# Optimization experiments

Measured on AMD Instinct MI355X. Metric: run time of the kernel, lower is better.

The kernel has to match this reference:

```python
import jax, jax.numpy as jnp
import numpy as np
import math

ROPE_BASE = 10000.0

def _rope(x):
    # x: [B, H, S, D]; interleaved-pair LLaMA-style rotary embedding
    S, D = x.shape[-2], x.shape[-1]
    inv_freq = 1.0 / (ROPE_BASE ** (jnp.arange(0, D, 2, dtype=jnp.float32) / D))  # [D/2]
    ang = jnp.arange(S, dtype=jnp.float32)[:, None] * inv_freq[None, :]           # [S, D/2]
    cos, sin = jnp.cos(ang), jnp.sin(ang)
    x1, x2 = x[..., 0::2], x[..., 1::2]
    r1 = x1 * cos - x2 * sin
    r2 = x1 * sin + x2 * cos
    return jnp.stack([r1, r2], axis=-1).reshape(x.shape)

def setup_inputs() -> dict:
    key = jax.random.key(0)
    ks = jax.random.split(key, 5)
    B, S, E = 2, 2048, 2048
    scale = 1.0 / math.sqrt(E)
    return {
        "x": jax.random.normal(ks[0], (B, S, E), dtype=jnp.float32),
        "Wq": jax.random.normal(ks[1], (E, E), dtype=jnp.float32) * scale,
        "Wk": jax.random.normal(ks[2], (E, E), dtype=jnp.float32) * scale,
        "Wv": jax.random.normal(ks[3], (E, E), dtype=jnp.float32) * scale,
        "Wo": jax.random.normal(ks[4], (E, E), dtype=jnp.float32) * scale,
    }

def reference(x, Wq, Wk, Wv, Wo):
    B, S, E = x.shape
    H = 16
    D = E // H
    # projections (torch Linear: y = x @ W^T, weights stored [out, in])
    def proj(W):
        y = jnp.einsum('bse,oe->bso', x, W)
        return y.reshape(B, S, H, D).transpose(0, 2, 1, 3)  # [B,H,S,D]
    q, k, v = proj(Wq), proj(Wk), proj(Wv)
    q_rot, k_rot = _rope(q), _rope(k)
    scores = jnp.einsum('bhqd,bhkd->bhqk', q_rot, k_rot) / jnp.sqrt(jnp.float32(D))
    causal = jnp.tril(jnp.ones((S, S), dtype=bool))
    scores = jnp.where(causal[None, None], scores, -jnp.inf)
    attn = jax.nn.softmax(scores, axis=-1)
    out = jnp.einsum('bhqk,bhkd->bhqd', attn, v)
    out = out.transpose(0, 2, 1, 3).reshape(B, S, E)
    attn_out = jnp.einsum('bse,oe->bso', out, Wo)
    return (attn_out, k, v)
```

## Files before the change

kernel.cpp:

```cpp
#include <hip/hip_runtime.h>

typedef __attribute__((ext_vector_type(8))) short short8;
typedef __attribute__((ext_vector_type(4))) float floatx4;

#define B_ 2
#define S_ 2048
#define E_ 2048
#define H_ 16
#define D_ 128

#define NEG_S  (-3.0e4f)
#define LOG2E  1.4426950408889634f

__device__ inline float bf2f(unsigned short u) {
    union { unsigned int i; float f; } v; v.i = ((unsigned int)u) << 16; return v.f;
}
__device__ inline unsigned short f2bf(float f) {
    union { float f; unsigned int i; } v; v.f = f;
    unsigned int r = v.i + 0x7FFFu + ((v.i >> 16) & 1u);
    return (unsigned short)(r >> 16);
}

__device__ inline void gload_lds16(const void* g, void* l) {
    __builtin_amdgcn_global_load_lds((__attribute__((address_space(1))) void*)(void*)g,
                                     (__attribute__((address_space(3))) void*)l, 16, 0, 0);
}

__global__ void rope_tab(float* __restrict__ cosT, float* __restrict__ sinT) {
    int idx = blockIdx.x * 256 + threadIdx.x;
    int s = idx >> 6, j = idx & 63;
    float inv = exp2f(-(float)(2 * j) * (13.287712379549449f / 128.0f));
    float ang = (float)s * inv;
    cosT[idx] = cosf(ang);
    sinT[idx] = sinf(ang);
}

__global__ __launch_bounds__(256) void cvt_bf16(const float* __restrict__ in,
                                                unsigned short* __restrict__ out, int n8) {
    int i = blockIdx.x * 256 + threadIdx.x;
    if (i >= n8) return;
    float4 f0 = *(const float4*)(in + (size_t)i * 8);
    float4 f1 = *(const float4*)(in + (size_t)i * 8 + 4);
    unsigned short u[8] = {f2bf(f0.x), f2bf(f0.y), f2bf(f0.z), f2bf(f0.w),
                           f2bf(f1.x), f2bf(f1.y), f2bf(f1.z), f2bf(f1.w)};
    *(uint4*)(out + (size_t)i * 8) = *(uint4*)u;
}

__global__ __launch_bounds__(256) void prep_k(const float* __restrict__ K,
                                              unsigned short* __restrict__ Kr,
                                              const float* __restrict__ cosT,
                                              const float* __restrict__ sinT) {
    int idx = blockIdx.x * 256 + threadIdx.x;
    int g = idx & 15;
    int s = (idx >> 4) & (S_ - 1);
    const float* src = K + (size_t)idx * 8;
    float4 f0 = *(const float4*)src;
    float4 f1 = *(const float4*)(src + 4);
    float xs[8] = {f0.x, f0.y, f0.z, f0.w, f1.x, f1.y, f1.z, f1.w};
    unsigned short u[8];
    int jb = g * 4;
#pragma unroll
    for (int i = 0; i < 4; i++) {
        float c = cosT[s * 64 + jb + i], sn = sinT[s * 64 + jb + i];
        float x1 = xs[2 * i], x2 = xs[2 * i + 1];
        u[2 * i]     = f2bf(x1 * c - x2 * sn);
        u[2 * i + 1] = f2bf(x1 * sn + x2 * c);
    }
    *(uint4*)(Kr + (size_t)idx * 8) = *(uint4*)u;
}

__global__ __launch_bounds__(256) void prep_v(const float* __restrict__ V,
                                              unsigned short* __restrict__ Vt) {
    __shared__ unsigned short Ls[64][130];
    int bh = blockIdx.y;
    int s0 = blockIdx.x * 64;
    int t = threadIdx.x;
    const float* src = V + ((size_t)bh * S_ + s0) * D_;
#pragma unroll
    for (int it = 0; it < 4; it++) {
        int r = it * 16 + (t >> 4), d0 = (t & 15) * 8;
        float4 f0 = *(const float4*)&src[(size_t)r * D_ + d0];
        float4 f1 = *(const float4*)&src[(size_t)r * D_ + d0 + 4];
        unsigned short u[8] = {f2bf(f0.x), f2bf(f0.y), f2bf(f0.z), f2bf(f0.w),
                               f2bf(f1.x), f2bf(f1.y), f2bf(f1.z), f2bf(f1.w)};
#pragma unroll
        for (int i = 0; i < 8; i++) Ls[r][d0 + i] = u[i];
    }
    __syncthreads();
    unsigned short* dst = Vt + (size_t)bh * D_ * S_;
#pragma unroll
    for (int it = 0; it < 4; it++) {
        int d = it * 32 + (t >> 3), ss = (t & 7) * 8;
        unsigned short u[8];
#pragma unroll
        for (int i = 0; i < 8; i++) u[i] = Ls[ss + i][d];
        *(uint4*)&dst[(size_t)d * S_ + s0 + ss] = *(uint4*)u;
    }
}

__global__ __launch_bounds__(256) void gemm128(const unsigned short* __restrict__ A,
                                               const unsigned short* __restrict__ Bw,
                                               void* __restrict__ dst, int dstMode) {
    __shared__ __align__(16) unsigned short As[128][32];
    __shared__ __align__(16) unsigned short Bs[128][32];
    int t = threadIdx.x;
    int wave = t >> 6, lane = t & 63;
    int quad = lane >> 4, l16 = lane & 15;
    int wr = wave >> 1, wc = wave & 1;

    floatx4 acc[4][4];
#pragma unroll
    for (int m = 0; m < 4; m++)
#pragma unroll
        for (int n = 0; n < 4; n++) acc[m][n] = (floatx4)(0.f);

    int srow = lane >> 2;
    int sg = lane & 3;
    const size_t aRow0 = (size_t)blockIdx.x * 128;
    const size_t bRow0 = (size_t)blockIdx.y * 128;

    for (int k0 = 0; k0 < E_; k0 += 32) {
#pragma unroll
        for (int i = 0; i < 2; i++) {
            int lr = wave * 32 + i * 16 + srow;
            int gg = sg ^ ((lr >> 1) & 3);
            gload_lds16(A + (aRow0 + lr) * E_ + k0 + gg * 8, &As[wave * 32 + i * 16][0]);
            gload_lds16(Bw + (bRow0 + lr) * E_ + k0 + gg * 8, &Bs[wave * 32 + i * 16][0]);
        }
        __syncthreads();
        short8 af[4], bfr[4];
#pragma unroll
        for (int m = 0; m < 4; m++) {
            int r = wr * 64 + m * 16 + l16;
            af[m] = *(const short8*)((const char*)As + r * 64 + ((quad ^ ((r >> 1) & 3)) << 4));
        }
#pragma unroll
        for (int n = 0; n < 4; n++) {
            int r = wc * 64 + n * 16 + l16;
            bfr[n] = *(const short8*)((const char*)Bs + r * 64 + ((quad ^ ((r >> 1) & 3)) << 4));
        }
#pragma unroll
        for (int m = 0; m < 4; m++)
#pragma unroll
            for (int n = 0; n < 4; n++)
                acc[m][n] = __builtin_amdgcn_mfma_f32_16x16x32_bf16(af[m], bfr[n], acc[m][n], 0, 0, 0);
        __syncthreads();
    }
#pragma unroll
    for (int m = 0; m < 4; m++)
#pragma unroll
        for (int n = 0; n < 4; n++)
#pragma unroll
            for (int rr = 0; rr < 4; rr++) {
                int mg = (int)aRow0 + wr * 64 + m * 16 + quad * 4 + rr;
                int ng = (int)bRow0 + wc * 64 + n * 16 + l16;
                float val = acc[m][n][rr];
                if (dstMode == 0) {
                    ((float*)dst)[(size_t)mg * E_ + ng] = val;
                } else if (dstMode == 1) {
                    int b = mg >> 11, s = mg & 2047, h = ng >> 7, d = ng & 127;
                    ((float*)dst)[(((size_t)(b * H_ + h)) * S_ + s) * D_ + d] = val;
                } else {
                    ((unsigned short*)dst)[(size_t)mg * E_ + ng] = f2bf(val);
                }
            }
}

__global__ __launch_bounds__(256) void attn_fast(const unsigned short* __restrict__ Qf,
                                                 const unsigned short* __restrict__ Kr,
                                                 const unsigned short* __restrict__ Vt,
                                                 const float* __restrict__ cosT,
                                                 const float* __restrict__ sinT,
                                                 unsigned short* __restrict__ Omid) {
    __shared__ __align__(16) unsigned short Ks[64][128];
    __shared__ __align__(16) unsigned short Vs[128][64];
    __shared__ __align__(16) unsigned short Ps[4][16][72];

    int t = threadIdx.x;
    int wave = t >> 6, lane = t & 63;
    int quad = lane >> 4, l16 = lane & 15;
    int orig = blockIdx.x;
    int L = (orig & 7) * 64 + (orig >> 3);
    int h = L >> 5;
    int qtile = 31 - (L & 31);
    int b = blockIdx.y;

    const unsigned short* Qb = Qf + (size_t)b * S_ * E_;
    const unsigned short* Kh = Kr + ((size_t)(b * H_ + h)) * S_ * D_;
    const unsigned short* Vh = Vt + ((size_t)(b * H_ + h)) * D_ * S_;

    int sq = qtile * 64 + wave * 16 + l16;
    short8 qf[4];
#pragma unroll
    for (int ks = 0; ks < 4; ks++) {
        int d0 = ks * 32 + quad * 8;
        union { uint4 u4; unsigned short u[8]; } un;
        un.u4 = *(const uint4*)&Qb[(size_t)sq * E_ + h * D_ + d0];
#pragma unroll
        for (int i = 0; i < 4; i++) {
            int j = (d0 >> 1) + i;
            float c = cosT[sq * 64 + j], s = sinT[sq * 64 + j];
            float x1 = bf2f(un.u[2 * i]), x2 = bf2f(un.u[2 * i + 1]);
            un.u[2 * i] = f2bf(x1 * c - x2 * s);
            un.u[2 * i + 1] = f2bf(x1 * s + x2 * c);
        }
        qf[ks] = *(short8*)un.u;
    }

    floatx4 O[8];
#pragma unroll
    for (int i = 0; i < 8; i++) O[i] = (floatx4)(0.f);
    float mrow[4], lrow[4];
#pragma unroll
    for (int r = 0; r < 4; r++) { mrow[r] = NEG_S; lrow[r] = 0.f; }

    const float scale = 0.08838834764831845f;

    for (int kt = 0; kt <= qtile; kt++) {
#pragma unroll
        for (int i = 0; i < 4; i++) {
            int r = wave * 16 + i * 4 + (lane >> 4);
            int g = (lane & 15) ^ (r & 7);
            gload_lds16(&Kh[(size_t)(kt * 64 + r) * D_ + g * 8], &Ks[wave * 16 + i * 4][0]);
        }
#pragma unroll
        for (int i = 0; i < 4; i++) {
            int r = wave * 32 + i * 8 + (lane >> 3);
            int g = (lane & 7) ^ (r & 7);
            gload_lds16(&Vh[(size_t)r * S_ + kt * 64 + g * 8], &Vs[wave * 32 + i * 8][0]);
        }
        __syncthreads();

        floatx4 sc[4];
#pragma unroll
        for (int ct = 0; ct < 4; ct++) sc[ct] = (floatx4)(0.f);
#pragma unroll
        for (int ks = 0; ks < 4; ks++) {
#pragma unroll
            for (int ct = 0; ct < 4; ct++) {
                int r = ct * 16 + l16;
                short8 kf = *(const short8*)((const char*)Ks + r * 256 +
                                             ((((ks << 2) + quad) ^ (r & 7)) << 4));
                sc[ct] = __builtin_amdgcn_mfma_f32_16x16x32_bf16(qf[ks], kf, sc[ct], 0, 0, 0);
            }
        }
        int rowbase = qtile * 64 + wave * 16 + quad * 4;
#pragma unroll
        for (int ct = 0; ct < 4; ct++) {
            int col = kt * 64 + ct * 16 + l16;
#pragma unroll
            for (int rr = 0; rr < 4; rr++) {
                float x = sc[ct][rr] * scale;
                sc[ct][rr] = (col > rowbase + rr) ? NEG_S : x;
            }
        }
        float alpha[4];
#pragma unroll
        for (int rr = 0; rr < 4; rr++) {
            float mx = fmaxf(fmaxf(sc[0][rr], sc[1][rr]), fmaxf(sc[2][rr], sc[3][rr]));
            mx = fmaxf(mx, __shfl_xor(mx, 1));
            mx = fmaxf(mx, __shfl_xor(mx, 2));
            mx = fmaxf(mx, __shfl_xor(mx, 4));
            mx = fmaxf(mx, __shfl_xor(mx, 8));
            float mnew = fmaxf(mrow[rr], mx);
            alpha[rr] = exp2f((mrow[rr] - mnew) * LOG2E);
            mrow[rr] = mnew;
        }
#pragma unroll
        for (int rr = 0; rr < 4; rr++) {
            float ps = 0.f;
#pragma unroll
            for (int ct = 0; ct < 4; ct++) {
                float p = exp2f((sc[ct][rr] - mrow[rr]) * LOG2E);
                sc[ct][rr] = p;
                ps += p;
            }
            ps += __shfl_xor(ps, 1);
            ps += __shfl_xor(ps, 2);
            ps += __shfl_xor(ps, 4);
            ps += __shfl_xor(ps, 8);
            lrow[rr] = lrow[rr] * alpha[rr] + ps;
        }
#pragma unroll
        for (int c8 = 0; c8 < 8; c8++)
#pragma unroll
            for (int rr = 0; rr < 4; rr++) O[c8][rr] *= alpha[rr];

#pragma unroll
        for (int ct = 0; ct < 4; ct++)
#pragma unroll
            for (int rr = 0; rr < 4; rr++)
                Ps[wave][quad * 4 + rr][ct * 16 + l16] = f2bf(sc[ct][rr]);
        asm volatile("s_waitcnt lgkmcnt(0)" ::: "memory");
        __builtin_amdgcn_sched_barrier(0);

#pragma unroll
        for (int ka2 = 0; ka2 < 2; ka2++) {
            short8 pa = *(const short8*)&Ps[wave][l16][ka2 * 32 + quad * 8];
#pragma unroll
            for (int c8 = 0; c8 < 8; c8++) {
                int r = c8 * 16 + l16;
                short8 vf = *(const short8*)((const char*)Vs + r * 128 +
                                             ((((ka2 << 2) + quad) ^ (r & 7)) << 4));
                O[c8] = __builtin_amdgcn_mfma_f32_16x16x32_bf16(pa, vf, O[c8], 0, 0, 0);
            }
        }
        asm volatile("s_waitcnt lgkmcnt(0)" ::: "memory");
        __builtin_amdgcn_sched_barrier(0);
        __syncthreads();
    }

#pragma unroll
    for (int rr = 0; rr < 4; rr++) {
        float inv = 1.f / lrow[rr];
        int row = qtile * 64 + wave * 16 + quad * 4 + rr;
#pragma unroll
        for (int c8 = 0; c8 < 8; c8++) {
            int d = c8 * 16 + l16;
            Omid[((size_t)b * S_ + row) * E_ + h * D_ + d] = f2bf(O[c8][rr] * inv);
        }
    }
}


__global__ __launch_bounds__(256) void gemm_bt(const void* __restrict__ A,
                                               const float* __restrict__ Bw,
                                               void* __restrict__ dst,
                                               int aBf16, int dstMode) {
    __shared__ __align__(16) unsigned short As[64][40];
    __shared__ __align__(16) unsigned short Bs[64][40];
    int t = threadIdx.x;
    int wave = t >> 6, lane = t & 63;
    int quad = lane >> 4, l16 = lane & 15;
    floatx4 acc[4];
#pragma unroll
    for (int i = 0; i < 4; i++) acc[i] = (floatx4)(0.f);

    int r = t >> 2, kc = (t & 3) * 8;
    int ra = blockIdx.x * 64 + r;
    int rb = blockIdx.y * 64 + r;

    for (int k0 = 0; k0 < E_; k0 += 32) {
        if (aBf16) {
            const unsigned short* Ab = (const unsigned short*)A + (size_t)ra * E_ + kc + k0;
            *(uint4*)&As[r][kc] = *(const uint4*)Ab;
        } else {
            const float* Af = (const float*)A + (size_t)ra * E_ + kc + k0;
            float4 f0 = *(const float4*)Af;
            float4 f1 = *(const float4*)(Af + 4);
            unsigned short u[8] = {f2bf(f0.x), f2bf(f0.y), f2bf(f0.z), f2bf(f0.w),
                                   f2bf(f1.x), f2bf(f1.y), f2bf(f1.z), f2bf(f1.w)};
            *(uint4*)&As[r][kc] = *(uint4*)u;
        }
        {
            const float* Bf = Bw + (size_t)rb * E_ + kc + k0;
            float4 g0 = *(const float4*)Bf;
            float4 g1 = *(const float4*)(Bf + 4);
            unsigned short u[8] = {f2bf(g0.x), f2bf(g0.y), f2bf(g0.z), f2bf(g0.w),
                                   f2bf(g1.x), f2bf(g1.y), f2bf(g1.z), f2bf(g1.w)};
            *(uint4*)&Bs[r][kc] = *(uint4*)u;
        }
        __syncthreads();
        short8 a = *(const short8*)&As[wave * 16 + l16][quad * 8];
#pragma unroll
        for (int ct = 0; ct < 4; ct++) {
            short8 bfr = *(const short8*)&Bs[ct * 16 + l16][quad * 8];
            acc[ct] = __builtin_amdgcn_mfma_f32_16x16x32_bf16(a, bfr, acc[ct], 0, 0, 0);
        }
        __syncthreads();
    }
#pragma unroll
    for (int ct = 0; ct < 4; ct++) {
#pragma unroll
        for (int rr = 0; rr < 4; rr++) {
            int m = blockIdx.x * 64 + wave * 16 + quad * 4 + rr;
            int n = blockIdx.y * 64 + ct * 16 + l16;
            float val = acc[ct][rr];
            if (dstMode == 0) {
                ((float*)dst)[(size_t)m * E_ + n] = val;
            } else if (dstMode == 1) {
                int b = m >> 11, s = m & 2047, h = n >> 7, d = n & 127;
                ((float*)dst)[(((size_t)(b * H_ + h)) * S_ + s) * D_ + d] = val;
            } else {
                ((unsigned short*)dst)[(size_t)m * E_ + n] = f2bf(val);
            }
        }
    }
}

__global__ __launch_bounds__(256) void attn_fwd(const unsigned short* __restrict__ Qf,
                                                const float* __restrict__ Kb0,
                                                const float* __restrict__ Vb0,
                                                const float* __restrict__ cosT,
                                                const float* __restrict__ sinT,
                                                unsigned short* __restrict__ Omid,
                                                int qtile0) {
    __shared__ __align__(16) unsigned short Ks[64][136];
    __shared__ __align__(16) unsigned short Vt[128][72];
    __shared__ __align__(16) unsigned short Ps[4][16][72];

    int t = threadIdx.x;
    int wave = t >> 6, lane = t & 63;
    int quad = lane >> 4, l16 = lane & 15;
    int qtile = qtile0 + blockIdx.x, h = blockIdx.y;
    const float* Kb = Kb0 + (size_t)h * S_ * D_;
    const float* Vb = Vb0 + (size_t)h * S_ * D_;

    int sq = qtile * 64 + wave * 16 + l16;
    short8 qf[4];
#pragma unroll
    for (int ks = 0; ks < 4; ks++) {
        int d0 = ks * 32 + quad * 8;
        union { uint4 u4; unsigned short u[8]; } un;
        un.u4 = *(const uint4*)&Qf[(size_t)sq * E_ + h * D_ + d0];
#pragma unroll
        for (int i = 0; i < 4; i++) {
            int j = (d0 >> 1) + i;
            float c = cosT[sq * 64 + j], s = sinT[sq * 64 + j];
            float x1 = bf2f(un.u[2 * i]), x2 = bf2f(un.u[2 * i + 1]);
            un.u[2 * i] = f2bf(x1 * c - x2 * s);
            un.u[2 * i + 1] = f2bf(x1 * s + x2 * c);
        }
        qf[ks] = *(short8*)un.u;
    }

    floatx4 O[8];
#pragma unroll
    for (int i = 0; i < 8; i++) O[i] = (floatx4)(0.f);
    float mrow[4], lrow[4];
#pragma unroll
    for (int r = 0; r < 4; r++) { mrow[r] = NEG_S; lrow[r] = 0.f; }

    const float scale = 0.08838834764831845f;

    for (int kt = 0; kt <= qtile; kt++) {
        __syncthreads();
        int r = t >> 2;
#pragma unroll
        for (int it = 0; it < 4; it++) {
            int d0 = (t & 3) * 8 + it * 32;
            int sk = kt * 64 + r;
            float4 ka = *(const float4*)&Kb[(size_t)sk * D_ + d0];
            float4 kb2 = *(const float4*)&Kb[(size_t)sk * D_ + d0 + 4];
            float xs[8] = {ka.x, ka.y, ka.z, ka.w, kb2.x, kb2.y, kb2.z, kb2.w};
            unsigned short u[8];
#pragma unroll
            for (int i = 0; i < 4; i++) {
                int j = (d0 >> 1) + i;
                float c = cosT[sk * 64 + j], s = sinT[sk * 64 + j];
                float x1 = xs[2 * i], x2 = xs[2 * i + 1];
                u[2 * i]     = f2bf(x1 * c - x2 * s);
                u[2 * i + 1] = f2bf(x1 * s + x2 * c);
            }
            *(uint4*)&Ks[r][d0] = *(uint4*)u;
            float4 va = *(const float4*)&Vb[(size_t)sk * D_ + d0];
            float4 vb2 = *(const float4*)&Vb[(size_t)sk * D_ + d0 + 4];
            float vs[8] = {va.x, va.y, va.z, va.w, vb2.x, vb2.y, vb2.z, vb2.w};
#pragma unroll
            for (int i = 0; i < 8; i++) Vt[d0 + i][r] = f2bf(vs[i]);
        }
        __syncthreads();

        floatx4 sc[4];
#pragma unroll
        for (int ct = 0; ct < 4; ct++) sc[ct] = (floatx4)(0.f);
#pragma unroll
        for (int ks = 0; ks < 4; ks++) {
#pragma unroll
            for (int ct = 0; ct < 4; ct++) {
                short8 kf = *(const short8*)&Ks[ct * 16 + l16][ks * 32 + quad * 8];
                sc[ct] = __builtin_amdgcn_mfma_f32_16x16x32_bf16(qf[ks], kf, sc[ct], 0, 0, 0);
            }
        }
        int rowbase = qtile * 64 + wave * 16 + quad * 4;
#pragma unroll
        for (int ct = 0; ct < 4; ct++) {
            int col = kt * 64 + ct * 16 + l16;
#pragma unroll
            for (int rr = 0; rr < 4; rr++) {
                float x = sc[ct][rr] * scale;
                sc[ct][rr] = (col > rowbase + rr) ? NEG_S : x;
            }
        }
        float alpha[4];
#pragma unroll
        for (int rr = 0; rr < 4; rr++) {
            float mx = fmaxf(fmaxf(sc[0][rr], sc[1][rr]), fmaxf(sc[2][rr], sc[3][rr]));
            mx = fmaxf(mx, __shfl_xor(mx, 1));
            mx = fmaxf(mx, __shfl_xor(mx, 2));
            mx = fmaxf(mx, __shfl_xor(mx, 4));
            mx = fmaxf(mx, __shfl_xor(mx, 8));
            float mnew = fmaxf(mrow[rr], mx);
            alpha[rr] = exp2f((mrow[rr] - mnew) * LOG2E);
            mrow[rr] = mnew;
        }
#pragma unroll
        for (int rr = 0; rr < 4; rr++) {
            float ps = 0.f;
#pragma unroll
            for (int ct = 0; ct < 4; ct++) {
                float p = exp2f((sc[ct][rr] - mrow[rr]) * LOG2E);
                sc[ct][rr] = p;
                ps += p;
            }
            ps += __shfl_xor(ps, 1);
            ps += __shfl_xor(ps, 2);
            ps += __shfl_xor(ps, 4);
            ps += __shfl_xor(ps, 8);
            lrow[rr] = lrow[rr] * alpha[rr] + ps;
        }
#pragma unroll
        for (int c8 = 0; c8 < 8; c8++)
#pragma unroll
            for (int rr = 0; rr < 4; rr++) O[c8][rr] *= alpha[rr];

#pragma unroll
        for (int ct = 0; ct < 4; ct++)
#pragma unroll
            for (int rr = 0; rr < 4; rr++)
                Ps[wave][quad * 4 + rr][ct * 16 + l16] = f2bf(sc[ct][rr]);
        __syncthreads();

#pragma unroll
        for (int ka2 = 0; ka2 < 2; ka2++) {
            short8 pa = *(const short8*)&Ps[wave][l16][ka2 * 32 + quad * 8];
#pragma unroll
            for (int c8 = 0; c8 < 8; c8++) {
                short8 vf = *(const short8*)&Vt[c8 * 16 + l16][ka2 * 32 + quad * 8];
                O[c8] = __builtin_amdgcn_mfma_f32_16x16x32_bf16(pa, vf, O[c8], 0, 0, 0);
            }
        }
    }

#pragma unroll
    for (int rr = 0; rr < 4; rr++) {
        float inv = 1.f / lrow[rr];
        int lrw = blockIdx.x * 64 + wave * 16 + quad * 4 + rr;
#pragma unroll
        for (int c8 = 0; c8 < 8; c8++) {
            int d = c8 * 16 + l16;
            Omid[(size_t)lrw * E_ + h * D_ + d] = f2bf(O[c8][rr] * inv);
        }
    }
}

extern "C" void kernel_launch(void* const* d_in, const int* in_sizes, int n_in,
                              void* d_out, int out_size, void* d_ws, size_t ws_size,
                              hipStream_t stream) {
    const float* x  = (const float*)d_in[0];
    const float* Wq = (const float*)d_in[1];
    const float* Wk = (const float*)d_in[2];
    const float* Wv = (const float*)d_in[3];
    const float* Wo = (const float*)d_in[4];

    float* out_attn = (float*)d_out;
    float* out_k = out_attn + (size_t)B_ * H_ * S_ * D_;
    float* out_v = out_k + (size_t)B_ * H_ * S_ * D_;

    char* ws = (char*)d_ws;
    float* cosT = (float*)ws;
    float* sinT = cosT + S_ * (D_ / 2);
    size_t tab_bytes = 2u * S_ * (D_ / 2) * sizeof(float);

    size_t krBytes  = (size_t)B_ * H_ * S_ * D_ * 2;
    size_t wbBytes  = (size_t)E_ * E_ * 2;
    size_t midBytes = (size_t)B_ * S_ * E_ * 2;
    size_t needFast = tab_bytes + 2 * krBytes + wbBytes + midBytes;

    hipLaunchKernelGGL(rope_tab, dim3(512), dim3(256), 0, stream, cosT, sinT);

    if (ws_size >= needFast) {
        unsigned short* Kr  = (unsigned short*)(ws + tab_bytes);
        unsigned short* Vt  = Kr + (size_t)B_ * H_ * S_ * D_;
        unsigned short* Wb  = Vt + (size_t)B_ * H_ * S_ * D_;
        unsigned short* mid = Wb + (size_t)E_ * E_;
        unsigned short* xb    = (unsigned short*)out_attn;
        unsigned short* q_tmp = (unsigned short*)(out_attn + (size_t)S_ * E_);

        hipLaunchKernelGGL(cvt_bf16, dim3(4096), dim3(256), 0, stream, x, xb, 1048576);

        hipLaunchKernelGGL(cvt_bf16, dim3(2048), dim3(256), 0, stream, Wq, Wb, 524288);
        hipLaunchKernelGGL(gemm128, dim3(32, 16), dim3(256), 0, stream, xb, Wb, (void*)q_tmp, 3);

        hipLaunchKernelGGL(cvt_bf16, dim3(2048), dim3(256), 0, stream, Wk, Wb, 524288);
        hipLaunchKernelGGL(gemm128, dim3(32, 16), dim3(256), 0, stream, xb, Wb, (void*)out_k, 1);
        hipLaunchKernelGGL(prep_k, dim3(4096), dim3(256), 0, stream, out_k, Kr, cosT, sinT);

        hipLaunchKernelGGL(cvt_bf16, dim3(2048), dim3(256), 0, stream, Wv, Wb, 524288);
        hipLaunchKernelGGL(gemm128, dim3(32, 16), dim3(256), 0, stream, xb, Wb, (void*)out_v, 1);
        hipLaunchKernelGGL(prep_v, dim3(32, 32), dim3(256), 0, stream, out_v, Vt);

        hipLaunchKernelGGL(cvt_bf16, dim3(2048), dim3(256), 0, stream, Wo, Wb, 524288);

        hipLaunchKernelGGL(attn_fast, dim3(512, B_), dim3(256), 0, stream,
                           q_tmp, Kr, Vt, cosT, sinT, mid);
        hipLaunchKernelGGL(gemm128, dim3(32, 16), dim3(256), 0, stream, mid, Wb,
                           (void*)out_attn, 0);
    } else {
        unsigned short* q_tmp = (unsigned short*)(out_attn + (size_t)S_ * E_);
        unsigned short* mid = (unsigned short*)(ws + tab_bytes);
        size_t avail = ws_size > tab_bytes ? ws_size - tab_bytes : 0;
        int R = 64;
        for (int r = 2048; r >= 64; r >>= 1) {
            if ((size_t)r * E_ * 2 <= avail) { R = r; break; }
        }

        dim3 gg(64, 32);
        hipLaunchKernelGGL(gemm_bt, gg, dim3(256), 0, stream, (const void*)x, Wq, (void*)q_tmp, 0, 3);
        hipLaunchKernelGGL(gemm_bt, gg, dim3(256), 0, stream, (const void*)x, Wk, (void*)out_k, 0, 1);
        hipLaunchKernelGGL(gemm_bt, gg, dim3(256), 0, stream, (const void*)x, Wv, (void*)out_v, 0, 1);

        const size_t bhsd = (size_t)H_ * S_ * D_;
        for (int b = 0; b < B_; b++) {
            const unsigned short* qb = q_tmp + (size_t)b * S_ * E_;
            for (int c = 0; c < S_ / 64; c += R / 64) {
                hipLaunchKernelGGL(attn_fwd, dim3(R / 64, H_), dim3(256), 0, stream,
                                   qb, out_k + b * bhsd, out_v + b * bhsd,
                                   cosT, sinT, mid, c);
                hipLaunchKernelGGL(gemm_bt, dim3(R / 64, 32), dim3(256), 0, stream,
                                   (const void*)mid, Wo,
                                   (void*)(out_attn + ((size_t)b * S_ + c * 64) * E_), 1, 0);
            }
        }
    }
}
```

Measured before the change: 570.9 us.

## Double-buffer K/V tiles and process two query sub-tiles per attention block

The attention kernel now handles 128 query rows per block as two 64-row fragments that share each loaded K/V tile. K/V loads go through a two-stage LDS buffer, so the next tile is fetched while the current one is computed. The grid drops from 1024 to 512 blocks, with an XCD-aware mapping of (head, batch, qtile) that pairs short and long causal tiles. MFMA sections are raised with s_setprio. This cuts K/V traffic and barrier stalls, at the cost of more registers and LDS per block, lower occupancy, and a little extra masked work on the diagonal tiles.

```diff
diff --git a/kernel.cpp b/kernel.cpp
--- a/kernel.cpp
+++ b/kernel.cpp
@@ -166,160 +166,195 @@
             }
 }
 
-__global__ __launch_bounds__(256) void attn_fast(const unsigned short* __restrict__ Qf,
-                                                 const unsigned short* __restrict__ Kr,
-                                                 const unsigned short* __restrict__ Vt,
-                                                 const float* __restrict__ cosT,
-                                                 const float* __restrict__ sinT,
-                                                 unsigned short* __restrict__ Omid) {
-    __shared__ __align__(16) unsigned short Ks[64][128];
-    __shared__ __align__(16) unsigned short Vs[128][64];
+__global__ __launch_bounds__(256) void attn_fast2(const unsigned short* __restrict__ Qf,
+                                                  const unsigned short* __restrict__ Kr,
+                                                  const unsigned short* __restrict__ Vt,
+                                                  const float* __restrict__ cosT,
+                                                  const float* __restrict__ sinT,
+                                                  unsigned short* __restrict__ Omid) {
+    __shared__ __align__(16) unsigned short Ks[2][64][128];
+    __shared__ __align__(16) unsigned short Vs[2][128][64];
     __shared__ __align__(16) unsigned short Ps[4][16][72];
 
     int t = threadIdx.x;
     int wave = t >> 6, lane = t & 63;
     int quad = lane >> 4, l16 = lane & 15;
+
     int orig = blockIdx.x;
-    int L = (orig & 7) * 64 + (orig >> 3);
-    int h = L >> 5;
-    int qtile = 31 - (L & 31);
-    int b = blockIdx.y;
+    int xcd = orig & 7, slot = orig >> 3;
+    int G = xcd * 4 + (slot >> 4);
+    int h = G >> 1, b = G & 1;
+    int qr = slot & 15;
+    int qt = ((slot >> 5) & 1) ? (15 - qr) : qr;
 
     const unsigned short* Qb = Qf + (size_t)b * S_ * E_;
     const unsigned short* Kh = Kr + ((size_t)(b * H_ + h)) * S_ * D_;
     const unsigned short* Vh = Vt + ((size_t)(b * H_ + h)) * D_ * S_;
 
-    int sq = qtile * 64 + wave * 16 + l16;
-    short8 qf[4];
-#pragma unroll
-    for (int ks = 0; ks < 4; ks++) {
-        int d0 = ks * 32 + quad * 8;
-        union { uint4 u4; unsigned short u[8]; } un;
-        un.u4 = *(const uint4*)&Qb[(size_t)sq * E_ + h * D_ + d0];
-#pragma unroll
-        for (int i = 0; i < 4; i++) {
-            int j = (d0 >> 1) + i;
-            float c = cosT[sq * 64 + j], s = sinT[sq * 64 + j];
-            float x1 = bf2f(un.u[2 * i]), x2 = bf2f(un.u[2 * i + 1]);
-            un.u[2 * i] = f2bf(x1 * c - x2 * s);
-            un.u[2 * i + 1] = f2bf(x1 * s + x2 * c);
-        }
-        qf[ks] = *(short8*)un.u;
-    }
-
-    floatx4 O[8];
-#pragma unroll
-    for (int i = 0; i < 8; i++) O[i] = (floatx4)(0.f);
-    float mrow[4], lrow[4];
-#pragma unroll
-    for (int r = 0; r < 4; r++) { mrow[r] = NEG_S; lrow[r] = 0.f; }
+    short8 qf[2][4];
+#pragma unroll
+    for (int f = 0; f < 2; f++) {
+        int sq = qt * 128 + f * 64 + wave * 16 + l16;
+#pragma unroll
+        for (int ks = 0; ks < 4; ks++) {
+            int d0 = ks * 32 + quad * 8;
+            union { uint4 u4; unsigned short u[8]; } un;
+            un.u4 = *(const uint4*)&Qb[(size_t)sq * E_ + h * D_ + d0];
+#pragma unroll
+            for (int i = 0; i < 4; i++) {
+                int j = (d0 >> 1) + i;
+                float c = cosT[sq * 64 + j], s = sinT[sq * 64 + j];
+                float x1 = bf2f(un.u[2 * i]), x2 = bf2f(un.u[2 * i + 1]);
+                un.u[2 * i] = f2bf(x1 * c - x2 * s);
+                un.u[2 * i + 1] = f2bf(x1 * s + x2 * c);
+            }
+            qf[f][ks] = *(short8*)un.u;
+        }
+    }
+
+    floatx4 O[2][8];
+#pragma unroll
+    for (int f = 0; f < 2; f++)
+#pragma unroll
+        for (int i = 0; i < 8; i++) O[f][i] = (floatx4)(0.f);
+    float mrow[2][4], lrow[2][4];
+#pragma unroll
+    for (int f = 0; f < 2; f++)
+#pragma unroll
+        for (int r = 0; r < 4; r++) { mrow[f][r] = NEG_S; lrow[f][r] = 0.f; }
 
     const float scale = 0.08838834764831845f;
-
-    for (int kt = 0; kt <= qtile; kt++) {
-#pragma unroll
-        for (int i = 0; i < 4; i++) {
-            int r = wave * 16 + i * 4 + (lane >> 4);
-            int g = (lane & 15) ^ (r & 7);
-            gload_lds16(&Kh[(size_t)(kt * 64 + r) * D_ + g * 8], &Ks[wave * 16 + i * 4][0]);
-        }
-#pragma unroll
-        for (int i = 0; i < 4; i++) {
-            int r = wave * 32 + i * 8 + (lane >> 3);
-            int g = (lane & 7) ^ (r & 7);
-            gload_lds16(&Vh[(size_t)r * S_ + kt * 64 + g * 8], &Vs[wave * 32 + i * 8][0]);
-        }
-        __syncthreads();
-
-        floatx4 sc[4];
-#pragma unroll
-        for (int ct = 0; ct < 4; ct++) sc[ct] = (floatx4)(0.f);
+    int NT = 2 * qt + 2;
+
+#define STAGE(BUF, KT)                                                          \
+    {                                                                           \
+        _Pragma("unroll")                                                       \
+        for (int i_ = 0; i_ < 4; i_++) {                                        \
+            int r_ = wave * 16 + i_ * 4 + (lane >> 4);                          \
+            int g_ = (lane & 15) ^ (r_ & 7);                                    \
+            gload_lds16(&Kh[(size_t)((KT) * 64 + r_) * D_ + g_ * 8],            \
+                        &Ks[BUF][wave * 16 + i_ * 4][0]);                       \
+        }                                                                       \
+        _Pragma("unroll")                                                       \
+        for (int i_ = 0; i_ < 4; i_++) {                                        \
+            int r_ = wave * 32 + i_ * 8 + (lane >> 3);                          \
+            int g_ = (lane & 7) ^ (r_ & 7);                                     \
+            gload_lds16(&Vh[(size_t)r_ * S_ + (KT) * 64 + g_ * 8],              \
+                        &Vs[BUF][wave * 32 + i_ * 8][0]);                       \
+        }                                                                       \
+    }
+
+    STAGE(0, 0);
+    __syncthreads();
+
+    for (int kt = 0; kt < NT; kt++) {
+        int cur = kt & 1;
+        if (kt + 1 < NT) STAGE(cur ^ 1, kt + 1);
+
+        floatx4 sc[2][4];
+#pragma unroll
+        for (int f = 0; f < 2; f++)
+#pragma unroll
+            for (int ct = 0; ct < 4; ct++) sc[f][ct] = (floatx4)(0.f);
+        __builtin_amdgcn_s_setprio(1);
 #pragma unroll
         for (int ks = 0; ks < 4; ks++) {
 #pragma unroll
             for (int ct = 0; ct < 4; ct++) {
                 int r = ct * 16 + l16;
-                short8 kf = *(const short8*)((const char*)Ks + r * 256 +
+                short8 kf = *(const short8*)((const char*)&Ks[cur][0][0] + r * 256 +
                                              ((((ks << 2) + quad) ^ (r & 7)) << 4));
-                sc[ct] = __builtin_amdgcn_mfma_f32_16x16x32_bf16(qf[ks], kf, sc[ct], 0, 0, 0);
-            }
-        }
-        int rowbase = qtile * 64 + wave * 16 + quad * 4;
-#pragma unroll
-        for (int ct = 0; ct < 4; ct++) {
-            int col = kt * 64 + ct * 16 + l16;
+                sc[0][ct] = __builtin_amdgcn_mfma_f32_16x16x32_bf16(qf[0][ks], kf, sc[0][ct], 0, 0, 0);
+                sc[1][ct] = __builtin_amdgcn_mfma_f32_16x16x32_bf16(qf[1][ks], kf, sc[1][ct], 0, 0, 0);
+            }
+        }
+        __builtin_amdgcn_s_setprio(0);
+
+#pragma unroll
+        for (int f = 0; f < 2; f++) {
+            int rowbase = qt * 128 + f * 64 + wave * 16 + quad * 4;
+#pragma unroll
+            for (int ct = 0; ct < 4; ct++) {
+                int col = kt * 64 + ct * 16 + l16;
+#pragma unroll
+                for (int rr = 0; rr < 4; rr++) {
+                    float x = sc[f][ct][rr] * scale;
+                    sc[f][ct][rr] = (col > rowbase + rr) ? NEG_S : x;
+                }
+            }
+            float alpha[4];
 #pragma unroll
             for (int rr = 0; rr < 4; rr++) {
-                float x = sc[ct][rr] * scale;
-                sc[ct][rr] = (col > rowbase + rr) ? NEG_S : x;
-            }
-        }
-        float alpha[4];
+                float mx = fmaxf(fmaxf(sc[f][0][rr], sc[f][1][rr]),
+                                 fmaxf(sc[f][2][rr], sc[f][3][rr]));
+                mx = fmaxf(mx, __shfl_xor(mx, 1));
+                mx = fmaxf(mx, __shfl_xor(mx, 2));
+                mx = fmaxf(mx, __shfl_xor(mx, 4));
+                mx = fmaxf(mx, __shfl_xor(mx, 8));
+                float mnew = fmaxf(mrow[f][rr], mx);
+                alpha[rr] = exp2f((mrow[f][rr] - mnew) * LOG2E);
+                mrow[f][rr] = mnew;
+            }
+#pragma unroll
+            for (int rr = 0; rr < 4; rr++) {
+                float ps = 0.f;
+#pragma unroll
+                for (int ct = 0; ct < 4; ct++) {
+                    float p = exp2f((sc[f][ct][rr] - mrow[f][rr]) * LOG2E);
+                    sc[f][ct][rr] = p;
+                    ps += p;
+                }
+                ps += __shfl_xor(ps, 1);
+                ps += __shfl_xor(ps, 2);
+                ps += __shfl_xor(ps, 4);
+                ps += __shfl_xor(ps, 8);
+                lrow[f][rr] = lrow[f][rr] * alpha[rr] + ps;
+            }
+#pragma unroll
+            for (int c8 = 0; c8 < 8; c8++)
+#pragma unroll
+                for (int rr = 0; rr < 4; rr++) O[f][c8][rr] *= alpha[rr];
+
+            asm volatile("s_waitcnt lgkmcnt(0)" ::: "memory");
+            __builtin_amdgcn_sched_barrier(0);
+#pragma unroll
+            for (int ct = 0; ct < 4; ct++)
+#pragma unroll
+                for (int rr = 0; rr < 4; rr++)
+                    Ps[wave][quad * 4 + rr][ct * 16 + l16] = f2bf(sc[f][ct][rr]);
+            asm volatile("s_waitcnt lgkmcnt(0)" ::: "memory");
+            __builtin_amdgcn_sched_barrier(0);
+
+            __builtin_amdgcn_s_setprio(1);
+#pragma unroll
+            for (int ka2 = 0; ka2 < 2; ka2++) {
+                short8 pa = *(const short8*)&Ps[wave][l16][ka2 * 32 + quad * 8];
+#pragma unroll
+                for (int c8 = 0; c8 < 8; c8++) {
+                    int r = c8 * 16 + l16;
+                    short8 vf = *(const short8*)((const char*)&Vs[cur][0][0] + r * 128 +
+                                                 ((((ka2 << 2) + quad) ^ (r & 7)) << 4));
+                    O[f][c8] = __builtin_amdgcn_mfma_f32_16x16x32_bf16(pa, vf, O[f][c8], 0, 0, 0);
+                }
+            }
+            __builtin_amdgcn_s_setprio(0);
+        }
+        __syncthreads();
+    }
+#undef STAGE
+
+#pragma unroll
+    for (int f = 0; f < 2; f++)
 #pragma unroll
         for (int rr = 0; rr < 4; rr++) {
-            float mx = fmaxf(fmaxf(sc[0][rr], sc[1][rr]), fmaxf(sc[2][rr], sc[3][rr]));
-            mx = fmaxf(mx, __shfl_xor(mx, 1));
-            mx = fmaxf(mx, __shfl_xor(mx, 2));
-            mx = fmaxf(mx, __shfl_xor(mx, 4));
-            mx = fmaxf(mx, __shfl_xor(mx, 8));
-            float mnew = fmaxf(mrow[rr], mx);
-            alpha[rr] = exp2f((mrow[rr] - mnew) * LOG2E);
-            mrow[rr] = mnew;
-        }
-#pragma unroll
-        for (int rr = 0; rr < 4; rr++) {
-            float ps = 0.f;
-#pragma unroll
-            for (int ct = 0; ct < 4; ct++) {
-                float p = exp2f((sc[ct][rr] - mrow[rr]) * LOG2E);
-                sc[ct][rr] = p;
-                ps += p;
-            }
-            ps += __shfl_xor(ps, 1);
-            ps += __shfl_xor(ps, 2);
-            ps += __shfl_xor(ps, 4);
-            ps += __shfl_xor(ps, 8);
-            lrow[rr] = lrow[rr] * alpha[rr] + ps;
-        }
-#pragma unroll
-        for (int c8 = 0; c8 < 8; c8++)
-#pragma unroll
-            for (int rr = 0; rr < 4; rr++) O[c8][rr] *= alpha[rr];
-
-#pragma unroll
-        for (int ct = 0; ct < 4; ct++)
-#pragma unroll
-            for (int rr = 0; rr < 4; rr++)
-                Ps[wave][quad * 4 + rr][ct * 16 + l16] = f2bf(sc[ct][rr]);
-        asm volatile("s_waitcnt lgkmcnt(0)" ::: "memory");
-        __builtin_amdgcn_sched_barrier(0);
-
-#pragma unroll
-        for (int ka2 = 0; ka2 < 2; ka2++) {
-            short8 pa = *(const short8*)&Ps[wave][l16][ka2 * 32 + quad * 8];
+            float inv = 1.f / lrow[f][rr];
+            int row = qt * 128 + f * 64 + wave * 16 + quad * 4 + rr;
 #pragma unroll
             for (int c8 = 0; c8 < 8; c8++) {
-                int r = c8 * 16 + l16;
-                short8 vf = *(const short8*)((const char*)Vs + r * 128 +
-                                             ((((ka2 << 2) + quad) ^ (r & 7)) << 4));
-                O[c8] = __builtin_amdgcn_mfma_f32_16x16x32_bf16(pa, vf, O[c8], 0, 0, 0);
-            }
-        }
-        asm volatile("s_waitcnt lgkmcnt(0)" ::: "memory");
-        __builtin_amdgcn_sched_barrier(0);
-        __syncthreads();
-    }
-
-#pragma unroll
-    for (int rr = 0; rr < 4; rr++) {
-        float inv = 1.f / lrow[rr];
-        int row = qtile * 64 + wave * 16 + quad * 4 + rr;
-#pragma unroll
-        for (int c8 = 0; c8 < 8; c8++) {
-            int d = c8 * 16 + l16;
-            Omid[((size_t)b * S_ + row) * E_ + h * D_ + d] = f2bf(O[c8][rr] * inv);
-        }
-    }
+                int d = c8 * 16 + l16;
+                Omid[((size_t)b * S_ + row) * E_ + h * D_ + d] = f2bf(O[f][c8][rr] * inv);
+            }
+        }
 }
 
 
@@ -592,7 +627,7 @@
 
         hipLaunchKernelGGL(cvt_bf16, dim3(2048), dim3(256), 0, stream, Wo, Wb, 524288);
 
-        hipLaunchKernelGGL(attn_fast, dim3(512, B_), dim3(256), 0, stream,
+        hipLaunchKernelGGL(attn_fast2, dim3(512), dim3(256), 0, stream,
                            q_tmp, Kr, Vt, cosT, sinT, mid);
         hipLaunchKernelGGL(gemm128, dim3(32, 16), dim3(256), 0, stream, mid, Wb,
                            (void*)out_attn, 0);
```

Result: slower. 622.9 us (+9.1%).
